# Kernel tuning notes

Measured on AMD Instinct MI355X. Metric: run time of the kernel, lower is better.

The kernel has to match this reference:

```python
import jax, jax.numpy as jnp
import numpy as np

N, E, G = 100000, 400000, 2000   # nodes, edges, graphs
IN, H = 48, 128                  # in_channels, hidden_channels (= out_channels)
L = 6                            # num GIN layers
EPS = 1e-5                       # BatchNorm eps
SLOPE = 0.01                     # leaky_relu negative slope


def setup_inputs() -> dict:
    key = jax.random.key(0)
    ks = jax.random.split(key, 12)
    x = jax.random.normal(ks[0], (N, IN), jnp.float32)
    edge_index = jax.random.randint(ks[1], (2, E), 0, N)
    edge_attr = jax.random.normal(ks[2], (E, 4), jnp.float32)  # ignored by GINConv
    # sorted graph-assignment vector; guarantee every graph has >=1 node
    batch = jnp.sort(jnp.concatenate([jnp.arange(G),
                                      jax.random.randint(ks[3], (N - G,), 0, G)]))
    s = 0.05
    W1a = jax.random.normal(ks[4], (IN, H), jnp.float32) * s        # layer-0 MLP lin1
    W1b = jax.random.normal(ks[5], (L - 1, H, H), jnp.float32) * s  # layers 1..5 MLP lin1
    b1 = jnp.zeros((L, H), jnp.float32)
    g1 = jnp.ones((L, H), jnp.float32)    # inner BN scale
    be1 = jnp.zeros((L, H), jnp.float32)  # inner BN bias
    W2 = jax.random.normal(ks[6], (L, H, H), jnp.float32) * s       # MLP lin2
    b2 = jnp.zeros((L, H), jnp.float32)
    gn = jnp.ones((L - 1, H), jnp.float32)    # outer BN scale (layers 0..4)
    bn_b = jnp.zeros((L - 1, H), jnp.float32) # outer BN bias
    fc_w = jax.random.normal(ks[7], (2 * H, 64), jnp.float32) * s
    fc_b = jnp.zeros((64,), jnp.float32)
    fc2_w = jax.random.normal(ks[8], (64, 3), jnp.float32) * s
    fc2_b = jnp.zeros((3,), jnp.float32)
    return dict(x=x, edge_attr=edge_attr, W1a=W1a, W1b=W1b, b1=b1, g1=g1, be1=be1,
                W2=W2, b2=b2, gn=gn, bn_b=bn_b, fc_w=fc_w, fc_b=fc_b,
                fc2_w=fc2_w, fc2_b=fc2_b, edge_index=edge_index, batch=batch,
                num_graphs=G)


def _bn(h, g, b):
    # training-mode BatchNorm1d over node dim (biased variance, as torch)
    m = jnp.mean(h, axis=0)
    v = jnp.mean((h - m) ** 2, axis=0)
    return g * (h - m) * jax.lax.rsqrt(v + EPS) + b


def _lrelu(h):
    return jnp.where(h >= 0, h, SLOPE * h)


def reference(x, edge_attr, W1a, W1b, b1, g1, be1, W2, b2, gn, bn_b,
              fc_w, fc_b, fc2_w, fc2_b, edge_index, batch, num_graphs):
    del edge_attr  # GINConv does not use edge attributes
    src, dst = edge_index[0], edge_index[1]
    n = x.shape[0]
    h = x
    for l in range(L):
        # GINConv: (1 + eps) * x + sum_{j in N(i)} x_j, eps = 0
        agg = jax.ops.segment_sum(h[src], dst, num_segments=n)
        z = h + agg
        W1 = W1a if l == 0 else W1b[l - 1]
        # MLP([in, H, H]) with inner BatchNorm + leaky_relu, plain last linear
        z = _lrelu(_bn(z @ W1 + b1[l], g1[l], be1[l])) @ W2[l] + b2[l]
        if l < L - 1:  # outer norm + act, skipped on last layer
            z = _lrelu(_bn(z, gn[l], bn_b[l]))
        h = z
    # dual global pooling over ragged per-graph segments
    cnt = jax.ops.segment_sum(jnp.ones((n, 1), h.dtype), batch, num_segments=num_graphs)
    p1 = jax.ops.segment_sum(h, batch, num_segments=num_graphs) / jnp.maximum(cnt, 1.0)
    p2 = jax.ops.segment_max(h, batch, num_segments=num_graphs)
    emb = jnp.concatenate([p1, p2], axis=1)            # [G, 256]
    out = _lrelu(emb @ fc_w + fc_b) @ fc2_w + fc2_b    # [G, 3]
    return out, emb
```

## Files before the change

kernel.cpp:

```cpp
#include <hip/hip_runtime.h>
#include <stdint.h>

#define N_NODES 100000
#define N_EDGES 400000
#define N_GRAPHS 2000
#define C_IN 48
#define HD 128
#define NLAYERS 6
#define BN_EPS 1e-5f
#define NSLOPE 0.01f
#define SB 391
#define NREP 8

typedef uint16_t u16;
typedef uint32_t u32;
typedef short bf16x8 __attribute__((ext_vector_type(8)));
typedef float f32x4 __attribute__((ext_vector_type(4)));

__device__ __forceinline__ float bf2f_lo(u32 v) { return __uint_as_float(v << 16); }
__device__ __forceinline__ float bf2f_hi(u32 v) { return __uint_as_float(v & 0xffff0000u); }
__device__ __forceinline__ float bf2f(u16 h) { return __uint_as_float(((u32)h) << 16); }
__device__ __forceinline__ u16 f2bf(float f) {
    u32 u = __float_as_uint(f);
    u32 r = (u + 0x7fffu + ((u >> 16) & 1u)) >> 16;
    return (u16)r;
}
__device__ __forceinline__ u32 pack2(float a, float b) {
    return (u32)f2bf(a) | ((u32)f2bf(b) << 16);
}
__device__ __forceinline__ float lrelu(float v) { return v >= 0.f ? v : v * NSLOPE; }

__global__ __launch_bounds__(256) void detect_kernel(const u16* __restrict__ x, int* __restrict__ mode) {
    __shared__ int flag;
    if (threadIdx.x == 0) flag = 0;
    __syncthreads();
    int local = 0;
    for (int i = threadIdx.x; i < 16384; i += 256) {
        float a = fabsf(bf2f(x[i]));
        if (!(a < 1e4f)) local = 1;
    }
    if (local) flag = 1;
    __syncthreads();
    if (threadIdx.x == 0) mode[0] = flag;
}

__global__ __launch_bounds__(256) void hist_kernel(const int* __restrict__ dst, int* __restrict__ cnt) {
    int e = blockIdx.x * 256 + threadIdx.x;
    if (e < N_EDGES) atomicAdd(&cnt[dst[e]], 1);
}

__global__ __launch_bounds__(256) void scan1_kernel(const int* __restrict__ cnt, int* __restrict__ bsum) {
    __shared__ int s[256];
    const int t = threadIdx.x;
    const int i = blockIdx.x * 256 + t;
    s[t] = (i < N_NODES) ? cnt[i] : 0;
    __syncthreads();
    for (int d = 128; d > 0; d >>= 1) {
        if (t < d) s[t] += s[t + d];
        __syncthreads();
    }
    if (t == 0) bsum[blockIdx.x] = s[0];
}

__global__ __launch_bounds__(512) void scan2_kernel(int* __restrict__ bsum, int* __restrict__ row_ptr) {
    __shared__ int s[SB];
    const int t = threadIdx.x;
    if (t < SB) s[t] = bsum[t];
    __syncthreads();
    if (t == 0) {
        int run = 0;
        for (int b = 0; b < SB; ++b) { int v = s[b]; s[b] = run; run += v; }
        row_ptr[0] = 0;
    }
    __syncthreads();
    if (t < SB) bsum[t] = s[t];
}

__global__ __launch_bounds__(256) void scan3_kernel(const int* __restrict__ cnt, const int* __restrict__ bsum,
                                                    int* __restrict__ row_ptr) {
    __shared__ int s[256];
    const int t = threadIdx.x;
    const int i = blockIdx.x * 256 + t;
    s[t] = (i < N_NODES) ? cnt[i] : 0;
    __syncthreads();
    if (t == 0) {
        int run = bsum[blockIdx.x];
        for (int j = 0; j < 256; ++j) { run += s[j]; s[j] = run; }
    }
    __syncthreads();
    if (i < N_NODES) row_ptr[i + 1] = s[t];
}

__global__ __launch_bounds__(256) void fill_kernel(const int* __restrict__ src, const int* __restrict__ dst,
                                                   int* __restrict__ cursor, int* __restrict__ col_idx) {
    int e = blockIdx.x * 256 + threadIdx.x;
    if (e < N_EDGES) {
        int d = dst[e];
        int slot = atomicAdd(&cursor[d], 1);
        col_idx[slot] = src[e];
    }
}

__global__ __launch_bounds__(256) void pack_w_kernel(const void* __restrict__ W1a, const void* __restrict__ W1b,
                                                     const void* __restrict__ W2, const int* __restrict__ mode,
                                                     u16* __restrict__ wpack) {
    const int t = blockIdx.x * 256 + threadIdx.x;
    if (t >= 24576) return;
    const int mat = t >> 11;
    const int r = t & 2047;
    const int l = r & 63;
    const int f = r >> 6;
    const int kb = f >> 3, nt = f & 7;
    const int k0 = kb * 32 + (l >> 4) * 8;
    const int n = nt * 16 + (l & 15);
    const int md = *mode;
    u16 vals[8];
    #pragma unroll
    for (int j = 0; j < 8; ++j) {
        const int k = k0 + j;
        float v;
        if (mat == 0) {
            v = (k < C_IN) ? (md ? ((const float*)W1a)[k * HD + n] : bf2f(((const u16*)W1a)[k * HD + n])) : 0.f;
        } else if (mat < 6) {
            const size_t o = (size_t)(mat - 1) * HD * HD + (size_t)k * HD + n;
            v = md ? ((const float*)W1b)[o] : bf2f(((const u16*)W1b)[o]);
        } else {
            const size_t o = (size_t)(mat - 6) * HD * HD + (size_t)k * HD + n;
            v = md ? ((const float*)W2)[o] : bf2f(((const u16*)W2)[o]);
        }
        vals[j] = f2bf(v);
    }
    uint4 o;
    o.x = (u32)vals[0] | ((u32)vals[1] << 16);
    o.y = (u32)vals[2] | ((u32)vals[3] << 16);
    o.z = (u32)vals[4] | ((u32)vals[5] << 16);
    o.w = (u32)vals[6] | ((u32)vals[7] << 16);
    *reinterpret_cast<uint4*>(wpack + (size_t)t * 8) = o;
}

__global__ __launch_bounds__(256) void pack_b_kernel(const void* __restrict__ b1, const void* __restrict__ b2,
                                                     const int* __restrict__ mode, float* __restrict__ biasf) {
    const int i = blockIdx.x * 256 + threadIdx.x;
    if (i >= 12 * HD) return;
    const int mat = i >> 7, c = i & 127;
    const int md = *mode;
    float v;
    if (mat < 6) v = md ? ((const float*)b1)[mat * HD + c] : bf2f(((const u16*)b1)[mat * HD + c]);
    else         v = md ? ((const float*)b2)[(mat - 6) * HD + c] : bf2f(((const u16*)b2)[(mat - 6) * HD + c]);
    biasf[i] = v;
}

__device__ __forceinline__ void coef_to_lds(float* coefs, const float* __restrict__ instats,
                                            const void* __restrict__ gammav, const void* __restrict__ betav,
                                            size_t gelem, int md, int tid) {
    if (tid < 128) {
        float sm = 0.f, sq = 0.f;
        #pragma unroll
        for (int rep = 0; rep < NREP; ++rep) {
            sm += instats[rep * 256 + tid];
            sq += instats[rep * 256 + 128 + tid];
        }
        const float inv_n = 1.0f / (float)N_NODES;
        const float mean = sm * inv_n;
        const float var = fmaxf(sq * inv_n - mean * mean, 0.f);
        const float rs = rsqrtf(var + BN_EPS);
        const float g  = md ? ((const float*)gammav)[gelem + tid] : bf2f(((const u16*)gammav)[gelem + tid]);
        const float be = md ? ((const float*)betav)[gelem + tid]  : bf2f(((const u16*)betav)[gelem + tid]);
        const float A = g * rs;
        coefs[tid] = A;
        coefs[128 + tid] = be - A * mean;
    }
}

template <int TRANS, int STATS>
__global__ __launch_bounds__(256) void gemm_mfma(const u16* A, const u16* __restrict__ wp,
                                                 const float* __restrict__ biasf,
                                                 const float* __restrict__ instats,
                                                 const void* __restrict__ gammav, const void* __restrict__ betav,
                                                 size_t gelem, const int* __restrict__ mode,
                                                 u16* out, float* __restrict__ stats) {
    __shared__ u16 Asm[32][136];
    __shared__ float sred[2][128];
    __shared__ float sqred[2][128];
    __shared__ float coefs[256];
    const int tid = threadIdx.x;
    const int m0 = blockIdx.x * 32;
    const int rrow = tid >> 4;
    const int seg = tid & 15;

    if (TRANS) {
        coef_to_lds(coefs, instats, gammav, betav, gelem, *mode, tid);
        __syncthreads();
    }

    {
        float cA[8], cB[8];
        if (TRANS) {
            #pragma unroll
            for (int j = 0; j < 8; ++j) {
                cA[j] = coefs[seg * 8 + j];
                cB[j] = coefs[128 + seg * 8 + j];
            }
        }
        uint4 v[2];
        #pragma unroll
        for (int i = 0; i < 2; ++i) {
            const int gm = m0 + i * 16 + rrow;
            if (gm < N_NODES) v[i] = *reinterpret_cast<const uint4*>(A + (size_t)gm * HD + seg * 8);
            else { v[i].x = 0; v[i].y = 0; v[i].z = 0; v[i].w = 0; }
        }
        #pragma unroll
        for (int i = 0; i < 2; ++i) {
            uint4 o = v[i];
            if (TRANS) {
                u32 w[4] = {o.x, o.y, o.z, o.w};
                #pragma unroll
                for (int p = 0; p < 4; ++p) {
                    const float lo = lrelu(cA[2 * p] * bf2f_lo(w[p]) + cB[2 * p]);
                    const float hi = lrelu(cA[2 * p + 1] * bf2f_hi(w[p]) + cB[2 * p + 1]);
                    w[p] = pack2(lo, hi);
                }
                o.x = w[0]; o.y = w[1]; o.z = w[2]; o.w = w[3];
            }
            *reinterpret_cast<uint4*>(&Asm[i * 16 + rrow][seg * 8]) = o;
        }
    }
    __syncthreads();

    const int wave = tid >> 6, lane = tid & 63;
    const int quad = lane >> 4, lx = lane & 15;
    const int rowhalf = wave & 1;
    const int colhalf = wave >> 1;
    const int wrow = rowhalf * 16;
    f32x4 acc[4] = {};
    #pragma unroll
    for (int kb = 0; kb < 4; ++kb) {
        bf16x8 bfr[4];
        #pragma unroll
        for (int nt = 0; nt < 4; ++nt)
            bfr[nt] = *reinterpret_cast<const bf16x8*>(wp + (((size_t)(kb * 8 + colhalf * 4 + nt) * 64 + lane) << 3));
        const bf16x8 af = *reinterpret_cast<const bf16x8*>(&Asm[wrow + lx][kb * 32 + quad * 8]);
        #pragma unroll
        for (int nt = 0; nt < 4; ++nt)
            acc[nt] = __builtin_amdgcn_mfma_f32_16x16x32_bf16(af, bfr[nt], acc[nt], 0, 0, 0);
    }

    const int mrow0 = m0 + wrow;
    #pragma unroll
    for (int nt = 0; nt < 4; ++nt) {
        const int n = colhalf * 64 + nt * 16 + lx;
        const float bj = biasf[n];
        float s = 0.f, q = 0.f;
        #pragma unroll
        for (int r = 0; r < 4; ++r) {
            const int m = mrow0 + quad * 4 + r;
            if (m < N_NODES) {
                const float v = acc[nt][r] + bj;
                out[(size_t)m * HD + n] = f2bf(v);
                if (STATS) { s += v; q += v * v; }
            }
        }
        if (STATS) {
            s += __shfl_xor(s, 16); s += __shfl_xor(s, 32);
            q += __shfl_xor(q, 16); q += __shfl_xor(q, 32);
            if (quad == 0) { sred[rowhalf][n] = s; sqred[rowhalf][n] = q; }
        }
    }
    if (STATS) {
        __syncthreads();
        float* sdst = stats + (size_t)(blockIdx.x & (NREP - 1)) * 256;
        if (tid < 128) {
            atomicAdd(&sdst[tid], sred[0][tid] + sred[1][tid]);
        } else if (tid < 256) {
            const int c2 = tid - 128;
            atomicAdd(&sdst[128 + c2], sqred[0][c2] + sqred[1][c2]);
        }
    }
}

__global__ __launch_bounds__(256) void gemm_gather(const u16* __restrict__ U, const int* __restrict__ row_ptr,
                                                   const int* __restrict__ col_idx, const u16* __restrict__ wp,
                                                   const float* __restrict__ biasf,
                                                   const float* __restrict__ instats,
                                                   const void* __restrict__ gammav, const void* __restrict__ betav,
                                                   size_t gelem, const int* __restrict__ mode,
                                                   u16* __restrict__ out, float* __restrict__ stats) {
    __shared__ u16 Asm[16][136];
    __shared__ float sred[128];
    __shared__ float sqred[128];
    __shared__ float coefs[256];
    const int tid = threadIdx.x;
    const int m0 = blockIdx.x * 16;
    const int rrow = tid >> 4;
    const int seg = tid & 15;

    coef_to_lds(coefs, instats, gammav, betav, gelem, *mode, tid);
    __syncthreads();

    {
        float cA[8], cB[8];
        #pragma unroll
        for (int j = 0; j < 8; ++j) {
            cA[j] = coefs[seg * 8 + j];
            cB[j] = coefs[128 + seg * 8 + j];
        }
        const int gm = m0 + rrow;
        float a[8];
        #pragma unroll
        for (int j = 0; j < 8; ++j) a[j] = 0.f;
        if (gm < N_NODES) {
            const uint4 v = *reinterpret_cast<const uint4*>(U + (size_t)gm * HD + seg * 8);
            const u32 w[4] = {v.x, v.y, v.z, v.w};
            #pragma unroll
            for (int p = 0; p < 4; ++p) {
                a[2 * p]     = lrelu(cA[2 * p] * bf2f_lo(w[p]) + cB[2 * p]);
                a[2 * p + 1] = lrelu(cA[2 * p + 1] * bf2f_hi(w[p]) + cB[2 * p + 1]);
            }
            const int s = row_ptr[gm];
            const int deg = row_ptr[gm + 1] - s;
            for (int t = 0; t < deg; t += 2) {
                const int id0 = col_idx[s + t];
                const bool h1 = (t + 1) < deg;
                const int id1 = h1 ? col_idx[s + t + 1] : 0;
                const uint4 r0 = *reinterpret_cast<const uint4*>(U + (size_t)id0 * HD + seg * 8);
                uint4 r1; r1.x = r1.y = r1.z = r1.w = 0;
                if (h1) r1 = *reinterpret_cast<const uint4*>(U + (size_t)id1 * HD + seg * 8);
                const u32 w0[4] = {r0.x, r0.y, r0.z, r0.w};
                const u32 w1[4] = {r1.x, r1.y, r1.z, r1.w};
                #pragma unroll
                for (int p = 0; p < 4; ++p) {
                    a[2 * p]     += lrelu(cA[2 * p] * bf2f_lo(w0[p]) + cB[2 * p]);
                    a[2 * p + 1] += lrelu(cA[2 * p + 1] * bf2f_hi(w0[p]) + cB[2 * p + 1]);
                    if (h1) {
                        a[2 * p]     += lrelu(cA[2 * p] * bf2f_lo(w1[p]) + cB[2 * p]);
                        a[2 * p + 1] += lrelu(cA[2 * p + 1] * bf2f_hi(w1[p]) + cB[2 * p + 1]);
                    }
                }
            }
        }
        uint4 o;
        o.x = pack2(a[0], a[1]); o.y = pack2(a[2], a[3]);
        o.z = pack2(a[4], a[5]); o.w = pack2(a[6], a[7]);
        *reinterpret_cast<uint4*>(&Asm[rrow][seg * 8]) = o;
    }
    __syncthreads();

    const int wave = tid >> 6, lane = tid & 63;
    const int quad = lane >> 4, lx = lane & 15;
    f32x4 acc[2] = {};
    #pragma unroll
    for (int kb = 0; kb < 4; ++kb) {
        bf16x8 bfr[2];
        #pragma unroll
        for (int nt = 0; nt < 2; ++nt)
            bfr[nt] = *reinterpret_cast<const bf16x8*>(wp + (((size_t)(kb * 8 + wave * 2 + nt) * 64 + lane) << 3));
        const bf16x8 af = *reinterpret_cast<const bf16x8*>(&Asm[lx][kb * 32 + quad * 8]);
        #pragma unroll
        for (int nt = 0; nt < 2; ++nt)
            acc[nt] = __builtin_amdgcn_mfma_f32_16x16x32_bf16(af, bfr[nt], acc[nt], 0, 0, 0);
    }

    #pragma unroll
    for (int nt = 0; nt < 2; ++nt) {
        const int n = wave * 32 + nt * 16 + lx;
        const float bj = biasf[n];
        float s = 0.f, q = 0.f;
        #pragma unroll
        for (int r = 0; r < 4; ++r) {
            const int m = m0 + quad * 4 + r;
            if (m < N_NODES) {
                const float v = acc[nt][r] + bj;
                out[(size_t)m * HD + n] = f2bf(v);
                s += v; q += v * v;
            }
        }
        s += __shfl_xor(s, 16); s += __shfl_xor(s, 32);
        q += __shfl_xor(q, 16); q += __shfl_xor(q, 32);
        if (quad == 0) { sred[n] = s; sqred[n] = q; }
    }
    __syncthreads();
    float* sdst = stats + (size_t)(blockIdx.x & (NREP - 1)) * 256;
    if (tid < 128) {
        atomicAdd(&sdst[tid], sred[tid]);
    } else if (tid < 256) {
        const int c2 = tid - 128;
        atomicAdd(&sdst[128 + c2], sqred[c2]);
    }
}

__global__ __launch_bounds__(256) void gemm_gather0(const void* __restrict__ xv, const int* __restrict__ row_ptr,
                                                    const int* __restrict__ col_idx, const u16* __restrict__ wp,
                                                    const float* __restrict__ biasf, const int* __restrict__ mode,
                                                    u16* __restrict__ out, float* __restrict__ stats) {
    __shared__ u16 Asm[16][136];
    __shared__ float sred[128];
    __shared__ float sqred[128];
    const int tid = threadIdx.x;
    const int m0 = blockIdx.x * 16;
    const int rrow = tid >> 4;
    const int seg = tid & 15;
    const int md = *mode;
    const bool act = seg < 6;

    {
        const int gm = m0 + rrow;
        float a[8];
        #pragma unroll
        for (int j = 0; j < 8; ++j) a[j] = 0.f;
        if (gm < N_NODES && act) {
            if (md) {
                const float* xf = (const float*)xv + (size_t)gm * C_IN + seg * 8;
                const float4 v0 = reinterpret_cast<const float4*>(xf)[0];
                const float4 v1 = reinterpret_cast<const float4*>(xf)[1];
                a[0] = v0.x; a[1] = v0.y; a[2] = v0.z; a[3] = v0.w;
                a[4] = v1.x; a[5] = v1.y; a[6] = v1.z; a[7] = v1.w;
            } else {
                const uint4 v = *reinterpret_cast<const uint4*>((const u16*)xv + (size_t)gm * C_IN + seg * 8);
                const u32 w[4] = {v.x, v.y, v.z, v.w};
                #pragma unroll
                for (int p = 0; p < 4; ++p) { a[2 * p] = bf2f_lo(w[p]); a[2 * p + 1] = bf2f_hi(w[p]); }
            }
        }
        if (gm < N_NODES) {
            const int s = row_ptr[gm];
            const int deg = row_ptr[gm + 1] - s;
            for (int t = 0; t < deg; t += 2) {
                const int id0 = col_idx[s + t];
                const bool h1 = (t + 1) < deg;
                const int id1 = h1 ? col_idx[s + t + 1] : 0;
                if (act) {
                    if (md) {
                        const float* p0 = (const float*)xv + (size_t)id0 * C_IN + seg * 8;
                        const float4 u0 = reinterpret_cast<const float4*>(p0)[0];
                        const float4 u1 = reinterpret_cast<const float4*>(p0)[1];
                        a[0] += u0.x; a[1] += u0.y; a[2] += u0.z; a[3] += u0.w;
                        a[4] += u1.x; a[5] += u1.y; a[6] += u1.z; a[7] += u1.w;
                        if (h1) {
                            const float* p1 = (const float*)xv + (size_t)id1 * C_IN + seg * 8;
                            const float4 t0 = reinterpret_cast<const float4*>(p1)[0];
                            const float4 t1 = reinterpret_cast<const float4*>(p1)[1];
                            a[0] += t0.x; a[1] += t0.y; a[2] += t0.z; a[3] += t0.w;
                            a[4] += t1.x; a[5] += t1.y; a[6] += t1.z; a[7] += t1.w;
                        }
                    } else {
                        const uint4 r0 = *reinterpret_cast<const uint4*>((const u16*)xv + (size_t)id0 * C_IN + seg * 8);
                        const u32 w0[4] = {r0.x, r0.y, r0.z, r0.w};
                        #pragma unroll
                        for (int p = 0; p < 4; ++p) { a[2 * p] += bf2f_lo(w0[p]); a[2 * p + 1] += bf2f_hi(w0[p]); }
                        if (h1) {
                            const uint4 r1 = *reinterpret_cast<const uint4*>((const u16*)xv + (size_t)id1 * C_IN + seg * 8);
                            const u32 w1[4] = {r1.x, r1.y, r1.z, r1.w};
                            #pragma unroll
                            for (int p = 0; p < 4; ++p) { a[2 * p] += bf2f_lo(w1[p]); a[2 * p + 1] += bf2f_hi(w1[p]); }
                        }
                    }
                }
            }
        }
        uint4 o;
        o.x = pack2(a[0], a[1]); o.y = pack2(a[2], a[3]);
        o.z = pack2(a[4], a[5]); o.w = pack2(a[6], a[7]);
        *reinterpret_cast<uint4*>(&Asm[rrow][seg * 8]) = o;
    }
    __syncthreads();

    const int wave = tid >> 6, lane = tid & 63;
    const int quad = lane >> 4, lx = lane & 15;
    f32x4 acc[2] = {};
    #pragma unroll
    for (int kb = 0; kb < 4; ++kb) {
        bf16x8 bfr[2];
        #pragma unroll
        for (int nt = 0; nt < 2; ++nt)
            bfr[nt] = *reinterpret_cast<const bf16x8*>(wp + (((size_t)(kb * 8 + wave * 2 + nt) * 64 + lane) << 3));
        const bf16x8 af = *reinterpret_cast<const bf16x8*>(&Asm[lx][kb * 32 + quad * 8]);
        #pragma unroll
        for (int nt = 0; nt < 2; ++nt)
            acc[nt] = __builtin_amdgcn_mfma_f32_16x16x32_bf16(af, bfr[nt], acc[nt], 0, 0, 0);
    }

    #pragma unroll
    for (int nt = 0; nt < 2; ++nt) {
        const int n = wave * 32 + nt * 16 + lx;
        const float bj = biasf[n];
        float s = 0.f, q = 0.f;
        #pragma unroll
        for (int r = 0; r < 4; ++r) {
            const int m = m0 + quad * 4 + r;
            if (m < N_NODES) {
                const float v = acc[nt][r] + bj;
                out[(size_t)m * HD + n] = f2bf(v);
                s += v; q += v * v;
            }
        }
        s += __shfl_xor(s, 16); s += __shfl_xor(s, 32);
        q += __shfl_xor(q, 16); q += __shfl_xor(q, 32);
        if (quad == 0) { sred[n] = s; sqred[n] = q; }
    }
    __syncthreads();
    float* sdst = stats + (size_t)(blockIdx.x & (NREP - 1)) * 256;
    if (tid < 128) {
        atomicAdd(&sdst[tid], sred[tid]);
    } else if (tid < 256) {
        const int c2 = tid - 128;
        atomicAdd(&sdst[128 + c2], sqred[c2]);
    }
}

__global__ __launch_bounds__(256) void pool_kernel(const u16* __restrict__ hf, const int* __restrict__ batch,
                                                   const int* __restrict__ mode, float* __restrict__ emb,
                                                   void* __restrict__ outv) {
    const int wave = threadIdx.x >> 6, lane = threadIdx.x & 63;
    const int g = blockIdx.x * 4 + wave;
    if (g >= N_GRAPHS) return;
    const int md = *mode;
    const int quad = lane >> 4, c = lane & 15;
    int lo = 0, hi = N_NODES;
    while (lo < hi) { int m = (lo + hi) >> 1; if (batch[m] < g) lo = m + 1; else hi = m; }
    const int s = lo;
    hi = N_NODES;
    while (lo < hi) { int m = (lo + hi) >> 1; if (batch[m] < g + 1) lo = m + 1; else hi = m; }
    const int e = lo;
    const int cnt = e - s;
    float sum[8], mx[8];
    #pragma unroll
    for (int j = 0; j < 8; ++j) { sum[j] = 0.f; mx[j] = -INFINITY; }
    for (int n = s + quad; n < e; n += 4) {
        const uint4 v = *reinterpret_cast<const uint4*>(hf + (size_t)n * HD + c * 8);
        const u32 w[4] = {v.x, v.y, v.z, v.w};
        #pragma unroll
        for (int p = 0; p < 4; ++p) {
            const float f0 = bf2f_lo(w[p]), f1 = bf2f_hi(w[p]);
            sum[2 * p] += f0; sum[2 * p + 1] += f1;
            mx[2 * p] = fmaxf(mx[2 * p], f0); mx[2 * p + 1] = fmaxf(mx[2 * p + 1], f1);
        }
    }
    #pragma unroll
    for (int j = 0; j < 8; ++j) {
        sum[j] += __shfl_xor(sum[j], 16); sum[j] += __shfl_xor(sum[j], 32);
        mx[j] = fmaxf(mx[j], __shfl_xor(mx[j], 16));
        mx[j] = fmaxf(mx[j], __shfl_xor(mx[j], 32));
    }
    if (quad == 0) {
        const float invc = 1.0f / (float)max(cnt, 1);
        const size_t base = (size_t)N_GRAPHS * 3 + (size_t)g * 256;
        #pragma unroll
        for (int j = 0; j < 8; ++j) {
            const float mean = sum[j] * invc;
            const float m2 = (cnt == 0) ? 0.f : mx[j];
            const int col = c * 8 + j;
            emb[(size_t)g * 256 + col] = mean;
            emb[(size_t)g * 256 + 128 + col] = m2;
            if (md) {
                ((float*)outv)[base + col] = mean;
                ((float*)outv)[base + 128 + col] = m2;
            } else {
                ((u16*)outv)[base + col] = f2bf(mean);
                ((u16*)outv)[base + 128 + col] = f2bf(m2);
            }
        }
    }
}

__global__ __launch_bounds__(64) void final_kernel(const float* __restrict__ emb, const void* __restrict__ fcwv,
                                                   const void* __restrict__ fcbv, const void* __restrict__ fc2wv,
                                                   const void* __restrict__ fc2bv, const int* __restrict__ mode,
                                                   void* __restrict__ outv) {
    __shared__ float es[256];
    __shared__ float hs[64];
    const int g = blockIdx.x, t = threadIdx.x;
    const int md = *mode;
    reinterpret_cast<float4*>(es)[t] = reinterpret_cast<const float4*>(emb + (size_t)g * 256)[t];
    __syncthreads();
    float acc = md ? ((const float*)fcbv)[t] : bf2f(((const u16*)fcbv)[t]);
    if (md) {
        const float* w = (const float*)fcwv;
        #pragma unroll 8
        for (int k = 0; k < 256; ++k) acc += es[k] * w[k * 64 + t];
    } else {
        const u16* w = (const u16*)fcwv;
        #pragma unroll 8
        for (int k = 0; k < 256; ++k) acc += es[k] * bf2f(w[k * 64 + t]);
    }
    hs[t] = lrelu(acc);
    __syncthreads();
    if (t < 3) {
        float o = md ? ((const float*)fc2bv)[t] : bf2f(((const u16*)fc2bv)[t]);
        if (md) {
            const float* w = (const float*)fc2wv;
            #pragma unroll 8
            for (int j = 0; j < 64; ++j) o += hs[j] * w[j * 3 + t];
            ((float*)outv)[(size_t)g * 3 + t] = o;
        } else {
            const u16* w = (const u16*)fc2wv;
            #pragma unroll 8
            for (int j = 0; j < 64; ++j) o += hs[j] * bf2f(w[j * 3 + t]);
            ((u16*)outv)[(size_t)g * 3 + t] = f2bf(o);
        }
    }
}

static inline size_t align256(size_t x) { return (x + 255) & ~(size_t)255; }

extern "C" void kernel_launch(void* const* d_in, const int* in_sizes, int n_in,
                              void* d_out, int out_size, void* d_ws, size_t ws_size,
                              hipStream_t stream) {
    (void)in_sizes; (void)n_in; (void)out_size; (void)ws_size;
    const void* x    = d_in[0];
    const void* W1a  = d_in[2];
    const void* W1b  = d_in[3];
    const void* b1   = d_in[4];
    const void* g1   = d_in[5];
    const void* be1  = d_in[6];
    const void* W2   = d_in[7];
    const void* b2   = d_in[8];
    const void* gn   = d_in[9];
    const void* bnb  = d_in[10];
    const void* fcw  = d_in[11];
    const void* fcb  = d_in[12];
    const void* fc2w = d_in[13];
    const void* fc2b = d_in[14];
    const int* ei    = (const int*)d_in[15];
    const int* batch = (const int*)d_in[16];

    char* p = (char*)d_ws;
    size_t off = 0;
    u16* zb = (u16*)(p + off); off += align256((size_t)N_NODES * HD * 2);
    u16* hb = (u16*)(p + off); off += align256((size_t)N_NODES * HD * 2);
    u16* wpack = (u16*)(p + off); off += align256((size_t)12 * HD * HD * 2);
    float* biasf = (float*)(p + off); off += align256((size_t)12 * HD * 4);
    float* emb = (float*)(p + off); off += align256((size_t)N_GRAPHS * 256 * 4);
    int* row_ptr = (int*)(p + off); off += align256((size_t)(N_NODES + 1) * 4);
    int* cursor = (int*)(p + off); off += align256((size_t)N_NODES * 4);
    int* col_idx = (int*)(p + off); off += align256((size_t)N_EDGES * 4);
    int* bsum = (int*)(p + off); off += align256((size_t)SB * 4);
    float* statsAll = (float*)(p + off); off += align256((size_t)12 * NREP * 256 * 4);
    int* mode = (int*)(p + off); off += align256(4);

    const int EB = (N_EDGES + 255) / 256;
    const int GBM = (N_NODES + 31) / 32;
    const int GBG = (N_NODES + 15) / 16;

    detect_kernel<<<1, 256, 0, stream>>>((const u16*)x, mode);

    hipMemsetAsync(cursor, 0, (size_t)N_NODES * 4, stream);
    hipMemsetAsync(statsAll, 0, (size_t)12 * NREP * 256 * 4, stream);
    hist_kernel<<<EB, 256, 0, stream>>>(ei + N_EDGES, cursor);
    scan1_kernel<<<SB, 256, 0, stream>>>(cursor, bsum);
    scan2_kernel<<<1, 512, 0, stream>>>(bsum, row_ptr);
    scan3_kernel<<<SB, 256, 0, stream>>>(cursor, bsum, row_ptr);
    hipMemcpyAsync(cursor, row_ptr, (size_t)N_NODES * 4, hipMemcpyDeviceToDevice, stream);
    fill_kernel<<<EB, 256, 0, stream>>>(ei, ei + N_EDGES, cursor, col_idx);
    pack_w_kernel<<<96, 256, 0, stream>>>(W1a, W1b, W2, mode, wpack);
    pack_b_kernel<<<6, 256, 0, stream>>>(b1, b2, mode, biasf);

    u16* cur = zb;
    u16* oth = hb;
    for (int l = 0; l < NLAYERS; ++l) {
        float* statsA = statsAll + (size_t)l * NREP * 256;
        float* statsB = statsAll + (size_t)(6 + l) * NREP * 256;
        float* statsBprev = statsAll + (size_t)(6 + l - 1) * NREP * 256;
        if (l == 0) {
            gemm_gather0<<<GBG, 256, 0, stream>>>(x, row_ptr, col_idx, wpack,
                                                  biasf, mode, cur, statsA);
        } else {
            gemm_gather<<<GBG, 256, 0, stream>>>(cur, row_ptr, col_idx,
                                                 wpack + (size_t)l * HD * HD,
                                                 biasf + (size_t)l * HD, statsBprev, gn, bnb,
                                                 (size_t)(l - 1) * HD, mode, oth, statsA);
            u16* t = cur; cur = oth; oth = t;
        }
        if (l < NLAYERS - 1) {
            gemm_mfma<1, 1><<<GBM, 256, 0, stream>>>(cur, wpack + (size_t)(6 + l) * HD * HD,
                                                     biasf + (size_t)(6 + l) * HD, statsA, g1, be1,
                                                     (size_t)l * HD, mode, cur, statsB);
        } else {
            gemm_mfma<1, 0><<<GBM, 256, 0, stream>>>(cur, wpack + (size_t)(6 + l) * HD * HD,
                                                     biasf + (size_t)(6 + l) * HD, statsA, g1, be1,
                                                     (size_t)l * HD, mode, cur, nullptr);
        }
    }

    pool_kernel<<<(N_GRAPHS + 3) / 4, 256, 0, stream>>>(cur, batch, mode, emb, d_out);
    final_kernel<<<N_GRAPHS, 64, 0, stream>>>(emb, fcw, fcb, fc2w, fc2b, mode, d_out);
}
```

Before: 598.2 us.

## Process gather rows in degree-sorted order to balance work per block

Adds a counting-sort pass that builds a node permutation ordered by in-degree, and the fused gather+GEMM kernels process rows in that order so nodes of similar degree share a block and a wave. This is meant to reduce divergence and tail imbalance in the neighbor-gather loops. Outputs are scattered back to original row positions, so the stores are no longer contiguous. The change also rewrites the address arithmetic to 32-bit byte offsets and uses a max-based leaky ReLU. Three small setup kernels are added.

```diff
diff --git a/kernel.cpp b/kernel.cpp
--- a/kernel.cpp
+++ b/kernel.cpp
@@ -11,6 +11,7 @@
 #define NSLOPE 0.01f
 #define SB 391
 #define NREP 8
+#define DMAX 64
 
 typedef uint16_t u16;
 typedef uint32_t u32;
@@ -28,7 +29,7 @@
 __device__ __forceinline__ u32 pack2(float a, float b) {
     return (u32)f2bf(a) | ((u32)f2bf(b) << 16);
 }
-__device__ __forceinline__ float lrelu(float v) { return v >= 0.f ? v : v * NSLOPE; }
+__device__ __forceinline__ float lrelu(float v) { return fmaxf(v * NSLOPE, v); }
 
 __global__ __launch_bounds__(256) void detect_kernel(const u16* __restrict__ x, int* __restrict__ mode) {
     __shared__ int flag;
@@ -99,6 +100,48 @@
         int slot = atomicAdd(&cursor[d], 1);
         col_idx[slot] = src[e];
     }
+}
+
+__global__ __launch_bounds__(256) void dhist_kernel(const int* __restrict__ row_ptr, int* __restrict__ dh) {
+    __shared__ int lh[DMAX];
+    const int t = threadIdx.x;
+    if (t < DMAX) lh[t] = 0;
+    __syncthreads();
+    const int i = blockIdx.x * 256 + t;
+    if (i < N_NODES) {
+        int d = row_ptr[i + 1] - row_ptr[i];
+        if (d > DMAX - 1) d = DMAX - 1;
+        atomicAdd(&lh[d], 1);
+    }
+    __syncthreads();
+    if (t < DMAX && lh[t]) atomicAdd(&dh[t], lh[t]);
+}
+
+__global__ __launch_bounds__(64) void dscan_kernel(int* __restrict__ dh, int* __restrict__ dcur) {
+    if (threadIdx.x == 0) {
+        int run = 0;
+        for (int d = DMAX - 1; d >= 0; --d) { int v = dh[d]; dh[d] = run; dcur[d] = run; run += v; }
+    }
+}
+
+__global__ __launch_bounds__(256) void dscat_kernel(const int* __restrict__ row_ptr, int* __restrict__ dcur,
+                                                    int* __restrict__ perm) {
+    __shared__ int lh[DMAX];
+    __shared__ int lbase[DMAX];
+    const int t = threadIdx.x;
+    if (t < DMAX) lh[t] = 0;
+    __syncthreads();
+    const int i = blockIdx.x * 256 + t;
+    int d = 0, r = 0;
+    if (i < N_NODES) {
+        d = row_ptr[i + 1] - row_ptr[i];
+        if (d > DMAX - 1) d = DMAX - 1;
+        r = atomicAdd(&lh[d], 1);
+    }
+    __syncthreads();
+    if (t < DMAX) lbase[t] = lh[t] ? atomicAdd(&dcur[t], lh[t]) : 0;
+    __syncthreads();
+    if (i < N_NODES) perm[lbase[d] + r] = i;
 }
 
 __global__ __launch_bounds__(256) void pack_w_kernel(const void* __restrict__ W1a, const void* __restrict__ W1b,
@@ -279,7 +322,8 @@
 }
 
 __global__ __launch_bounds__(256) void gemm_gather(const u16* __restrict__ U, const int* __restrict__ row_ptr,
-                                                   const int* __restrict__ col_idx, const u16* __restrict__ wp,
+                                                   const int* __restrict__ col_idx, const int* __restrict__ perm,
+                                                   const u16* __restrict__ wp,
                                                    const float* __restrict__ biasf,
                                                    const float* __restrict__ instats,
                                                    const void* __restrict__ gammav, const void* __restrict__ betav,
@@ -304,17 +348,21 @@
             cA[j] = coefs[seg * 8 + j];
             cB[j] = coefs[128 + seg * 8 + j];
         }
-        const int gm = m0 + rrow;
+        const int gm0 = m0 + rrow;
+        const int gm = (gm0 < N_NODES) ? perm[gm0] : -1;
         float a[8];
         #pragma unroll
         for (int j = 0; j < 8; ++j) a[j] = 0.f;
-        if (gm < N_NODES) {
-            const uint4 v = *reinterpret_cast<const uint4*>(U + (size_t)gm * HD + seg * 8);
-            const u32 w[4] = {v.x, v.y, v.z, v.w};
-            #pragma unroll
-            for (int p = 0; p < 4; ++p) {
-                a[2 * p]     = lrelu(cA[2 * p] * bf2f_lo(w[p]) + cB[2 * p]);
-                a[2 * p + 1] = lrelu(cA[2 * p + 1] * bf2f_hi(w[p]) + cB[2 * p + 1]);
+        if (gm >= 0) {
+            const u32 soff = (u32)seg << 4;
+            {
+                const uint4 v = *reinterpret_cast<const uint4*>((const char*)U + (((u32)gm << 8) + soff));
+                const u32 w[4] = {v.x, v.y, v.z, v.w};
+                #pragma unroll
+                for (int p = 0; p < 4; ++p) {
+                    a[2 * p]     = lrelu(cA[2 * p] * bf2f_lo(w[p]) + cB[2 * p]);
+                    a[2 * p + 1] = lrelu(cA[2 * p + 1] * bf2f_hi(w[p]) + cB[2 * p + 1]);
+                }
             }
             const int s = row_ptr[gm];
             const int deg = row_ptr[gm + 1] - s;
@@ -322,9 +370,9 @@
                 const int id0 = col_idx[s + t];
                 const bool h1 = (t + 1) < deg;
                 const int id1 = h1 ? col_idx[s + t + 1] : 0;
-                const uint4 r0 = *reinterpret_cast<const uint4*>(U + (size_t)id0 * HD + seg * 8);
+                const uint4 r0 = *reinterpret_cast<const uint4*>((const char*)U + (((u32)id0 << 8) + soff));
                 uint4 r1; r1.x = r1.y = r1.z = r1.w = 0;
-                if (h1) r1 = *reinterpret_cast<const uint4*>(U + (size_t)id1 * HD + seg * 8);
+                if (h1) r1 = *reinterpret_cast<const uint4*>((const char*)U + (((u32)id1 << 8) + soff));
                 const u32 w0[4] = {r0.x, r0.y, r0.z, r0.w};
                 const u32 w1[4] = {r1.x, r1.y, r1.z, r1.w};
                 #pragma unroll
@@ -360,6 +408,12 @@
             acc[nt] = __builtin_amdgcn_mfma_f32_16x16x32_bf16(af, bfr[nt], acc[nt], 0, 0, 0);
     }
 
+    int pm[4];
+    #pragma unroll
+    for (int r = 0; r < 4; ++r) {
+        const int mm = m0 + quad * 4 + r;
+        pm[r] = (mm < N_NODES) ? perm[mm] : -1;
+    }
     #pragma unroll
     for (int nt = 0; nt < 2; ++nt) {
         const int n = wave * 32 + nt * 16 + lx;
@@ -367,10 +421,9 @@
         float s = 0.f, q = 0.f;
         #pragma unroll
         for (int r = 0; r < 4; ++r) {
-            const int m = m0 + quad * 4 + r;
-            if (m < N_NODES) {
+            if (pm[r] >= 0) {
                 const float v = acc[nt][r] + bj;
-                out[(size_t)m * HD + n] = f2bf(v);
+                out[(size_t)pm[r] * HD + n] = f2bf(v);
                 s += v; q += v * v;
             }
         }
@@ -389,7 +442,8 @@
 }
 
 __global__ __launch_bounds__(256) void gemm_gather0(const void* __restrict__ xv, const int* __restrict__ row_ptr,
-                                                    const int* __restrict__ col_idx, const u16* __restrict__ wp,
+                                                    const int* __restrict__ col_idx, const int* __restrict__ perm,
+                                                    const u16* __restrict__ wp,
                                                     const float* __restrict__ biasf, const int* __restrict__ mode,
                                                     u16* __restrict__ out, float* __restrict__ stats) {
     __shared__ u16 Asm[16][136];
@@ -403,56 +457,61 @@
     const bool act = seg < 6;
 
     {
-        const int gm = m0 + rrow;
+        const int gm0 = m0 + rrow;
+        const int gm = (gm0 < N_NODES) ? perm[gm0] : -1;
         float a[8];
         #pragma unroll
         for (int j = 0; j < 8; ++j) a[j] = 0.f;
-        if (gm < N_NODES && act) {
-            if (md) {
-                const float* xf = (const float*)xv + (size_t)gm * C_IN + seg * 8;
-                const float4 v0 = reinterpret_cast<const float4*>(xf)[0];
-                const float4 v1 = reinterpret_cast<const float4*>(xf)[1];
-                a[0] = v0.x; a[1] = v0.y; a[2] = v0.z; a[3] = v0.w;
-                a[4] = v1.x; a[5] = v1.y; a[6] = v1.z; a[7] = v1.w;
-            } else {
-                const uint4 v = *reinterpret_cast<const uint4*>((const u16*)xv + (size_t)gm * C_IN + seg * 8);
-                const u32 w[4] = {v.x, v.y, v.z, v.w};
-                #pragma unroll
-                for (int p = 0; p < 4; ++p) { a[2 * p] = bf2f_lo(w[p]); a[2 * p + 1] = bf2f_hi(w[p]); }
-            }
-        }
-        if (gm < N_NODES) {
+        if (gm >= 0 && act) {
             const int s = row_ptr[gm];
             const int deg = row_ptr[gm + 1] - s;
-            for (int t = 0; t < deg; t += 2) {
-                const int id0 = col_idx[s + t];
-                const bool h1 = (t + 1) < deg;
-                const int id1 = h1 ? col_idx[s + t + 1] : 0;
-                if (act) {
-                    if (md) {
-                        const float* p0 = (const float*)xv + (size_t)id0 * C_IN + seg * 8;
-                        const float4 u0 = reinterpret_cast<const float4*>(p0)[0];
-                        const float4 u1 = reinterpret_cast<const float4*>(p0)[1];
-                        a[0] += u0.x; a[1] += u0.y; a[2] += u0.z; a[3] += u0.w;
-                        a[4] += u1.x; a[5] += u1.y; a[6] += u1.z; a[7] += u1.w;
-                        if (h1) {
-                            const float* p1 = (const float*)xv + (size_t)id1 * C_IN + seg * 8;
-                            const float4 t0 = reinterpret_cast<const float4*>(p1)[0];
-                            const float4 t1 = reinterpret_cast<const float4*>(p1)[1];
-                            a[0] += t0.x; a[1] += t0.y; a[2] += t0.z; a[3] += t0.w;
-                            a[4] += t1.x; a[5] += t1.y; a[6] += t1.z; a[7] += t1.w;
-                        }
-                    } else {
-                        const uint4 r0 = *reinterpret_cast<const uint4*>((const u16*)xv + (size_t)id0 * C_IN + seg * 8);
-                        const u32 w0[4] = {r0.x, r0.y, r0.z, r0.w};
+            if (md) {
+                const u32 soff = (u32)seg << 5;
+                {
+                    const char* pr = (const char*)xv + ((u32)gm * 192u + soff);
+                    const float4 v0 = reinterpret_cast<const float4*>(pr)[0];
+                    const float4 v1 = reinterpret_cast<const float4*>(pr)[1];
+                    a[0] = v0.x; a[1] = v0.y; a[2] = v0.z; a[3] = v0.w;
+                    a[4] = v1.x; a[5] = v1.y; a[6] = v1.z; a[7] = v1.w;
+                }
+                for (int t = 0; t < deg; t += 2) {
+                    const int id0 = col_idx[s + t];
+                    const bool h1 = (t + 1) < deg;
+                    const int id1 = h1 ? col_idx[s + t + 1] : 0;
+                    const char* p0 = (const char*)xv + ((u32)id0 * 192u + soff);
+                    const float4 u0 = reinterpret_cast<const float4*>(p0)[0];
+                    const float4 u1 = reinterpret_cast<const float4*>(p0)[1];
+                    a[0] += u0.x; a[1] += u0.y; a[2] += u0.z; a[3] += u0.w;
+                    a[4] += u1.x; a[5] += u1.y; a[6] += u1.z; a[7] += u1.w;
+                    if (h1) {
+                        const char* p1 = (const char*)xv + ((u32)id1 * 192u + soff);
+                        const float4 t0 = reinterpret_cast<const float4*>(p1)[0];
+                        const float4 t1 = reinterpret_cast<const float4*>(p1)[1];
+                        a[0] += t0.x; a[1] += t0.y; a[2] += t0.z; a[3] += t0.w;
+                        a[4] += t1.x; a[5] += t1.y; a[6] += t1.z; a[7] += t1.w;
+                    }
+                }
+            } else {
+                const u32 soff = (u32)seg << 4;
+                {
+                    const uint4 v = *reinterpret_cast<const uint4*>((const char*)xv + ((u32)gm * 96u + soff));
+                    const u32 w[4] = {v.x, v.y, v.z, v.w};
+                    #pragma unroll
+                    for (int p = 0; p < 4; ++p) { a[2 * p] = bf2f_lo(w[p]); a[2 * p + 1] = bf2f_hi(w[p]); }
+                }
+                for (int t = 0; t < deg; t += 2) {
+                    const int id0 = col_idx[s + t];
+                    const bool h1 = (t + 1) < deg;
+                    const int id1 = h1 ? col_idx[s + t + 1] : 0;
+                    const uint4 r0 = *reinterpret_cast<const uint4*>((const char*)xv + ((u32)id0 * 96u + soff));
+                    const u32 w0[4] = {r0.x, r0.y, r0.z, r0.w};
+                    #pragma unroll
+                    for (int p = 0; p < 4; ++p) { a[2 * p] += bf2f_lo(w0[p]); a[2 * p + 1] += bf2f_hi(w0[p]); }
+                    if (h1) {
+                        const uint4 r1 = *reinterpret_cast<const uint4*>((const char*)xv + ((u32)id1 * 96u + soff));
+                        const u32 w1[4] = {r1.x, r1.y, r1.z, r1.w};
                         #pragma unroll
-                        for (int p = 0; p < 4; ++p) { a[2 * p] += bf2f_lo(w0[p]); a[2 * p + 1] += bf2f_hi(w0[p]); }
-                        if (h1) {
-                            const uint4 r1 = *reinterpret_cast<const uint4*>((const u16*)xv + (size_t)id1 * C_IN + seg * 8);
-                            const u32 w1[4] = {r1.x, r1.y, r1.z, r1.w};
-                            #pragma unroll
-                            for (int p = 0; p < 4; ++p) { a[2 * p] += bf2f_lo(w1[p]); a[2 * p + 1] += bf2f_hi(w1[p]); }
-                        }
+                        for (int p = 0; p < 4; ++p) { a[2 * p] += bf2f_lo(w1[p]); a[2 * p + 1] += bf2f_hi(w1[p]); }
                     }
                 }
             }
@@ -479,6 +538,12 @@
             acc[nt] = __builtin_amdgcn_mfma_f32_16x16x32_bf16(af, bfr[nt], acc[nt], 0, 0, 0);
     }
 
+    int pm[4];
+    #pragma unroll
+    for (int r = 0; r < 4; ++r) {
+        const int mm = m0 + quad * 4 + r;
+        pm[r] = (mm < N_NODES) ? perm[mm] : -1;
+    }
     #pragma unroll
     for (int nt = 0; nt < 2; ++nt) {
         const int n = wave * 32 + nt * 16 + lx;
@@ -486,10 +551,9 @@
         float s = 0.f, q = 0.f;
         #pragma unroll
         for (int r = 0; r < 4; ++r) {
-            const int m = m0 + quad * 4 + r;
-            if (m < N_NODES) {
+            if (pm[r] >= 0) {
                 const float v = acc[nt][r] + bj;
-                out[(size_t)m * HD + n] = f2bf(v);
+                out[(size_t)pm[r] * HD + n] = f2bf(v);
                 s += v; q += v * v;
             }
         }
@@ -635,6 +699,9 @@
     int* col_idx = (int*)(p + off); off += align256((size_t)N_EDGES * 4);
     int* bsum = (int*)(p + off); off += align256((size_t)SB * 4);
     float* statsAll = (float*)(p + off); off += align256((size_t)12 * NREP * 256 * 4);
+    int* perm = (int*)(p + off); off += align256((size_t)N_NODES * 4);
+    int* dh = (int*)(p + off); off += align256((size_t)DMAX * 4);
+    int* dcur = (int*)(p + off); off += align256((size_t)DMAX * 4);
     int* mode = (int*)(p + off); off += align256(4);
 
     const int EB = (N_EDGES + 255) / 256;
@@ -645,10 +712,14 @@
 
     hipMemsetAsync(cursor, 0, (size_t)N_NODES * 4, stream);
     hipMemsetAsync(statsAll, 0, (size_t)12 * NREP * 256 * 4, stream);
+    hipMemsetAsync(dh, 0, (size_t)DMAX * 4, stream);
     hist_kernel<<<EB, 256, 0, stream>>>(ei + N_EDGES, cursor);
     scan1_kernel<<<SB, 256, 0, stream>>>(cursor, bsum);
     scan2_kernel<<<1, 512, 0, stream>>>(bsum, row_ptr);
     scan3_kernel<<<SB, 256, 0, stream>>>(cursor, bsum, row_ptr);
+    dhist_kernel<<<SB, 256, 0, stream>>>(row_ptr, dh);
+    dscan_kernel<<<1, 64, 0, stream>>>(dh, dcur);
+    dscat_kernel<<<SB, 256, 0, stream>>>(row_ptr, dcur, perm);
     hipMemcpyAsync(cursor, row_ptr, (size_t)N_NODES * 4, hipMemcpyDeviceToDevice, stream);
     fill_kernel<<<EB, 256, 0, stream>>>(ei, ei + N_EDGES, cursor, col_idx);
     pack_w_kernel<<<96, 256, 0, stream>>>(W1a, W1b, W2, mode, wpack);
@@ -661,10 +732,10 @@
         float* statsB = statsAll + (size_t)(6 + l) * NREP * 256;
         float* statsBprev = statsAll + (size_t)(6 + l - 1) * NREP * 256;
         if (l == 0) {
-            gemm_gather0<<<GBG, 256, 0, stream>>>(x, row_ptr, col_idx, wpack,
+            gemm_gather0<<<GBG, 256, 0, stream>>>(x, row_ptr, col_idx, perm, wpack,
                                                   biasf, mode, cur, statsA);
         } else {
-            gemm_gather<<<GBG, 256, 0, stream>>>(cur, row_ptr, col_idx,
+            gemm_gather<<<GBG, 256, 0, stream>>>(cur, row_ptr, col_idx, perm,
                                                  wpack + (size_t)l * HD * HD,
                                                  biasf + (size_t)l * HD, statsBprev, gn, bnb,
                                                  (size_t)(l - 1) * HD, mode, oth, statsA);
```

Result: slower. 638.3 us (+6.7%).

## Shrink dense GEMM tile to 16 rows, drop bounds checks, use 32-bit offsets

Applied to the files above, without the earlier changes.

The dense MFMA GEMM now processes 16 rows per block instead of 32, with each wave owning 32 output columns. This doubles the grid size and halves per-wave accumulators. Row bounds checks are removed from all GEMM and gather kernels because N is divisible by 16. Address arithmetic switches to 32-bit byte offsets, and leaky ReLU becomes a max. The smaller tile costs twice as many weight fragment loads per row in exchange for more parallelism and fewer registers.

```diff
diff --git a/kernel.cpp b/kernel.cpp
--- a/kernel.cpp
+++ b/kernel.cpp
@@ -28,7 +28,7 @@
 __device__ __forceinline__ u32 pack2(float a, float b) {
     return (u32)f2bf(a) | ((u32)f2bf(b) << 16);
 }
-__device__ __forceinline__ float lrelu(float v) { return v >= 0.f ? v : v * NSLOPE; }
+__device__ __forceinline__ float lrelu(float v) { return fmaxf(v * NSLOPE, v); }
 
 __global__ __launch_bounds__(256) void detect_kernel(const u16* __restrict__ x, int* __restrict__ mode) {
     __shared__ int flag;
@@ -179,12 +179,12 @@
                                                  const void* __restrict__ gammav, const void* __restrict__ betav,
                                                  size_t gelem, const int* __restrict__ mode,
                                                  u16* out, float* __restrict__ stats) {
-    __shared__ u16 Asm[32][136];
-    __shared__ float sred[2][128];
-    __shared__ float sqred[2][128];
+    __shared__ u16 Asm[16][136];
+    __shared__ float sred[128];
+    __shared__ float sqred[128];
     __shared__ float coefs[256];
     const int tid = threadIdx.x;
-    const int m0 = blockIdx.x * 32;
+    const int m0 = blockIdx.x * 16;
     const int rrow = tid >> 4;
     const int seg = tid & 15;
 
@@ -194,86 +194,69 @@
     }
 
     {
-        float cA[8], cB[8];
+        const int gm = m0 + rrow;
+        uint4 o = *reinterpret_cast<const uint4*>((const char*)A + (((u32)gm << 8) + ((u32)seg << 4)));
         if (TRANS) {
+            float cA[8], cB[8];
             #pragma unroll
             for (int j = 0; j < 8; ++j) {
                 cA[j] = coefs[seg * 8 + j];
                 cB[j] = coefs[128 + seg * 8 + j];
             }
-        }
-        uint4 v[2];
-        #pragma unroll
-        for (int i = 0; i < 2; ++i) {
-            const int gm = m0 + i * 16 + rrow;
-            if (gm < N_NODES) v[i] = *reinterpret_cast<const uint4*>(A + (size_t)gm * HD + seg * 8);
-            else { v[i].x = 0; v[i].y = 0; v[i].z = 0; v[i].w = 0; }
-        }
-        #pragma unroll
-        for (int i = 0; i < 2; ++i) {
-            uint4 o = v[i];
-            if (TRANS) {
-                u32 w[4] = {o.x, o.y, o.z, o.w};
-                #pragma unroll
-                for (int p = 0; p < 4; ++p) {
-                    const float lo = lrelu(cA[2 * p] * bf2f_lo(w[p]) + cB[2 * p]);
-                    const float hi = lrelu(cA[2 * p + 1] * bf2f_hi(w[p]) + cB[2 * p + 1]);
-                    w[p] = pack2(lo, hi);
-                }
-                o.x = w[0]; o.y = w[1]; o.z = w[2]; o.w = w[3];
+            u32 w[4] = {o.x, o.y, o.z, o.w};
+            #pragma unroll
+            for (int p = 0; p < 4; ++p) {
+                const float lo = lrelu(cA[2 * p] * bf2f_lo(w[p]) + cB[2 * p]);
+                const float hi = lrelu(cA[2 * p + 1] * bf2f_hi(w[p]) + cB[2 * p + 1]);
+                w[p] = pack2(lo, hi);
             }
-            *reinterpret_cast<uint4*>(&Asm[i * 16 + rrow][seg * 8]) = o;
-        }
+            o.x = w[0]; o.y = w[1]; o.z = w[2]; o.w = w[3];
+        }
+        *reinterpret_cast<uint4*>(&Asm[rrow][seg * 8]) = o;
     }
     __syncthreads();
 
     const int wave = tid >> 6, lane = tid & 63;
     const int quad = lane >> 4, lx = lane & 15;
-    const int rowhalf = wave & 1;
-    const int colhalf = wave >> 1;
-    const int wrow = rowhalf * 16;
-    f32x4 acc[4] = {};
+    f32x4 acc[2] = {};
     #pragma unroll
     for (int kb = 0; kb < 4; ++kb) {
-        bf16x8 bfr[4];
-        #pragma unroll
-        for (int nt = 0; nt < 4; ++nt)
-            bfr[nt] = *reinterpret_cast<const bf16x8*>(wp + (((size_t)(kb * 8 + colhalf * 4 + nt) * 64 + lane) << 3));
-        const bf16x8 af = *reinterpret_cast<const bf16x8*>(&Asm[wrow + lx][kb * 32 + quad * 8]);
-        #pragma unroll
-        for (int nt = 0; nt < 4; ++nt)
+        bf16x8 bfr[2];
+        #pragma unroll
+        for (int nt = 0; nt < 2; ++nt)
+            bfr[nt] = *reinterpret_cast<const bf16x8*>(wp + (((size_t)(kb * 8 + wave * 2 + nt) * 64 + lane) << 3));
+        const bf16x8 af = *reinterpret_cast<const bf16x8*>(&Asm[lx][kb * 32 + quad * 8]);
+        #pragma unroll
+        for (int nt = 0; nt < 2; ++nt)
             acc[nt] = __builtin_amdgcn_mfma_f32_16x16x32_bf16(af, bfr[nt], acc[nt], 0, 0, 0);
     }
 
-    const int mrow0 = m0 + wrow;
-    #pragma unroll
-    for (int nt = 0; nt < 4; ++nt) {
-        const int n = colhalf * 64 + nt * 16 + lx;
+    #pragma unroll
+    for (int nt = 0; nt < 2; ++nt) {
+        const int n = wave * 32 + nt * 16 + lx;
         const float bj = biasf[n];
         float s = 0.f, q = 0.f;
         #pragma unroll
         for (int r = 0; r < 4; ++r) {
-            const int m = mrow0 + quad * 4 + r;
-            if (m < N_NODES) {
-                const float v = acc[nt][r] + bj;
-                out[(size_t)m * HD + n] = f2bf(v);
-                if (STATS) { s += v; q += v * v; }
-            }
+            const int m = m0 + quad * 4 + r;
+            const float v = acc[nt][r] + bj;
+            out[(size_t)m * HD + n] = f2bf(v);
+            if (STATS) { s += v; q += v * v; }
         }
         if (STATS) {
             s += __shfl_xor(s, 16); s += __shfl_xor(s, 32);
             q += __shfl_xor(q, 16); q += __shfl_xor(q, 32);
-            if (quad == 0) { sred[rowhalf][n] = s; sqred[rowhalf][n] = q; }
+            if (quad == 0) { sred[n] = s; sqred[n] = q; }
         }
     }
     if (STATS) {
         __syncthreads();
         float* sdst = stats + (size_t)(blockIdx.x & (NREP - 1)) * 256;
         if (tid < 128) {
-            atomicAdd(&sdst[tid], sred[0][tid] + sred[1][tid]);
+            atomicAdd(&sdst[tid], sred[tid]);
         } else if (tid < 256) {
             const int c2 = tid - 128;
-            atomicAdd(&sdst[128 + c2], sqred[0][c2] + sqred[1][c2]);
+            atomicAdd(&sdst[128 + c2], sqred[c2]);
         }
     }
 }
@@ -305,16 +288,19 @@
             cB[j] = coefs[128 + seg * 8 + j];
         }
         const int gm = m0 + rrow;
+        const u32 soff = (u32)seg << 4;
         float a[8];
         #pragma unroll
         for (int j = 0; j < 8; ++j) a[j] = 0.f;
-        if (gm < N_NODES) {
-            const uint4 v = *reinterpret_cast<const uint4*>(U + (size_t)gm * HD + seg * 8);
-            const u32 w[4] = {v.x, v.y, v.z, v.w};
-            #pragma unroll
-            for (int p = 0; p < 4; ++p) {
-                a[2 * p]     = lrelu(cA[2 * p] * bf2f_lo(w[p]) + cB[2 * p]);
-                a[2 * p + 1] = lrelu(cA[2 * p + 1] * bf2f_hi(w[p]) + cB[2 * p + 1]);
+        {
+            {
+                const uint4 v = *reinterpret_cast<const uint4*>((const char*)U + (((u32)gm << 8) + soff));
+                const u32 w[4] = {v.x, v.y, v.z, v.w};
+                #pragma unroll
+                for (int p = 0; p < 4; ++p) {
+                    a[2 * p]     = lrelu(cA[2 * p] * bf2f_lo(w[p]) + cB[2 * p]);
+                    a[2 * p + 1] = lrelu(cA[2 * p + 1] * bf2f_hi(w[p]) + cB[2 * p + 1]);
+                }
             }
             const int s = row_ptr[gm];
             const int deg = row_ptr[gm + 1] - s;
@@ -322,9 +308,9 @@
                 const int id0 = col_idx[s + t];
                 const bool h1 = (t + 1) < deg;
                 const int id1 = h1 ? col_idx[s + t + 1] : 0;
-                const uint4 r0 = *reinterpret_cast<const uint4*>(U + (size_t)id0 * HD + seg * 8);
+                const uint4 r0 = *reinterpret_cast<const uint4*>((const char*)U + (((u32)id0 << 8) + soff));
                 uint4 r1; r1.x = r1.y = r1.z = r1.w = 0;
-                if (h1) r1 = *reinterpret_cast<const uint4*>(U + (size_t)id1 * HD + seg * 8);
+                if (h1) r1 = *reinterpret_cast<const uint4*>((const char*)U + (((u32)id1 << 8) + soff));
                 const u32 w0[4] = {r0.x, r0.y, r0.z, r0.w};
                 const u32 w1[4] = {r1.x, r1.y, r1.z, r1.w};
                 #pragma unroll
@@ -368,11 +354,9 @@
         #pragma unroll
         for (int r = 0; r < 4; ++r) {
             const int m = m0 + quad * 4 + r;
-            if (m < N_NODES) {
-                const float v = acc[nt][r] + bj;
-                out[(size_t)m * HD + n] = f2bf(v);
-                s += v; q += v * v;
-            }
+            const float v = acc[nt][r] + bj;
+            out[(size_t)m * HD + n] = f2bf(v);
+            s += v; q += v * v;
         }
         s += __shfl_xor(s, 16); s += __shfl_xor(s, 32);
         q += __shfl_xor(q, 16); q += __shfl_xor(q, 32);
@@ -407,52 +391,56 @@
         float a[8];
         #pragma unroll
         for (int j = 0; j < 8; ++j) a[j] = 0.f;
-        if (gm < N_NODES && act) {
-            if (md) {
-                const float* xf = (const float*)xv + (size_t)gm * C_IN + seg * 8;
-                const float4 v0 = reinterpret_cast<const float4*>(xf)[0];
-                const float4 v1 = reinterpret_cast<const float4*>(xf)[1];
-                a[0] = v0.x; a[1] = v0.y; a[2] = v0.z; a[3] = v0.w;
-                a[4] = v1.x; a[5] = v1.y; a[6] = v1.z; a[7] = v1.w;
-            } else {
-                const uint4 v = *reinterpret_cast<const uint4*>((const u16*)xv + (size_t)gm * C_IN + seg * 8);
-                const u32 w[4] = {v.x, v.y, v.z, v.w};
-                #pragma unroll
-                for (int p = 0; p < 4; ++p) { a[2 * p] = bf2f_lo(w[p]); a[2 * p + 1] = bf2f_hi(w[p]); }
-            }
-        }
-        if (gm < N_NODES) {
+        if (act) {
             const int s = row_ptr[gm];
             const int deg = row_ptr[gm + 1] - s;
-            for (int t = 0; t < deg; t += 2) {
-                const int id0 = col_idx[s + t];
-                const bool h1 = (t + 1) < deg;
-                const int id1 = h1 ? col_idx[s + t + 1] : 0;
-                if (act) {
-                    if (md) {
-                        const float* p0 = (const float*)xv + (size_t)id0 * C_IN + seg * 8;
-                        const float4 u0 = reinterpret_cast<const float4*>(p0)[0];
-                        const float4 u1 = reinterpret_cast<const float4*>(p0)[1];
-                        a[0] += u0.x; a[1] += u0.y; a[2] += u0.z; a[3] += u0.w;
-                        a[4] += u1.x; a[5] += u1.y; a[6] += u1.z; a[7] += u1.w;
-                        if (h1) {
-                            const float* p1 = (const float*)xv + (size_t)id1 * C_IN + seg * 8;
-                            const float4 t0 = reinterpret_cast<const float4*>(p1)[0];
-                            const float4 t1 = reinterpret_cast<const float4*>(p1)[1];
-                            a[0] += t0.x; a[1] += t0.y; a[2] += t0.z; a[3] += t0.w;
-                            a[4] += t1.x; a[5] += t1.y; a[6] += t1.z; a[7] += t1.w;
-                        }
-                    } else {
-                        const uint4 r0 = *reinterpret_cast<const uint4*>((const u16*)xv + (size_t)id0 * C_IN + seg * 8);
-                        const u32 w0[4] = {r0.x, r0.y, r0.z, r0.w};
+            if (md) {
+                const u32 soff = (u32)seg << 5;
+                {
+                    const char* pr = (const char*)xv + ((u32)gm * 192u + soff);
+                    const float4 v0 = reinterpret_cast<const float4*>(pr)[0];
+                    const float4 v1 = reinterpret_cast<const float4*>(pr)[1];
+                    a[0] = v0.x; a[1] = v0.y; a[2] = v0.z; a[3] = v0.w;
+                    a[4] = v1.x; a[5] = v1.y; a[6] = v1.z; a[7] = v1.w;
+                }
+                for (int t = 0; t < deg; t += 2) {
+                    const int id0 = col_idx[s + t];
+                    const bool h1 = (t + 1) < deg;
+                    const int id1 = h1 ? col_idx[s + t + 1] : 0;
+                    const char* p0 = (const char*)xv + ((u32)id0 * 192u + soff);
+                    const float4 u0 = reinterpret_cast<const float4*>(p0)[0];
+                    const float4 u1 = reinterpret_cast<const float4*>(p0)[1];
+                    a[0] += u0.x; a[1] += u0.y; a[2] += u0.z; a[3] += u0.w;
+                    a[4] += u1.x; a[5] += u1.y; a[6] += u1.z; a[7] += u1.w;
+                    if (h1) {
+                        const char* p1 = (const char*)xv + ((u32)id1 * 192u + soff);
+                        const float4 t0 = reinterpret_cast<const float4*>(p1)[0];
+                        const float4 t1 = reinterpret_cast<const float4*>(p1)[1];
+                        a[0] += t0.x; a[1] += t0.y; a[2] += t0.z; a[3] += t0.w;
+                        a[4] += t1.x; a[5] += t1.y; a[6] += t1.z; a[7] += t1.w;
+                    }
+                }
+            } else {
+                const u32 soff = (u32)seg << 4;
+                {
+                    const uint4 v = *reinterpret_cast<const uint4*>((const char*)xv + ((u32)gm * 96u + soff));
+                    const u32 w[4] = {v.x, v.y, v.z, v.w};
+                    #pragma unroll
+                    for (int p = 0; p < 4; ++p) { a[2 * p] = bf2f_lo(w[p]); a[2 * p + 1] = bf2f_hi(w[p]); }
+                }
+                for (int t = 0; t < deg; t += 2) {
+                    const int id0 = col_idx[s + t];
+                    const bool h1 = (t + 1) < deg;
+                    const int id1 = h1 ? col_idx[s + t + 1] : 0;
+                    const uint4 r0 = *reinterpret_cast<const uint4*>((const char*)xv + ((u32)id0 * 96u + soff));
+                    const u32 w0[4] = {r0.x, r0.y, r0.z, r0.w};
+                    #pragma unroll
+                    for (int p = 0; p < 4; ++p) { a[2 * p] += bf2f_lo(w0[p]); a[2 * p + 1] += bf2f_hi(w0[p]); }
+                    if (h1) {
+                        const uint4 r1 = *reinterpret_cast<const uint4*>((const char*)xv + ((u32)id1 * 96u + soff));
+                        const u32 w1[4] = {r1.x, r1.y, r1.z, r1.w};
                         #pragma unroll
-                        for (int p = 0; p < 4; ++p) { a[2 * p] += bf2f_lo(w0[p]); a[2 * p + 1] += bf2f_hi(w0[p]); }
-                        if (h1) {
-                            const uint4 r1 = *reinterpret_cast<const uint4*>((const u16*)xv + (size_t)id1 * C_IN + seg * 8);
-                            const u32 w1[4] = {r1.x, r1.y, r1.z, r1.w};
-                            #pragma unroll
-                            for (int p = 0; p < 4; ++p) { a[2 * p] += bf2f_lo(w1[p]); a[2 * p + 1] += bf2f_hi(w1[p]); }
-                        }
+                        for (int p = 0; p < 4; ++p) { a[2 * p] += bf2f_lo(w1[p]); a[2 * p + 1] += bf2f_hi(w1[p]); }
                     }
                 }
             }
@@ -487,11 +475,9 @@
         #pragma unroll
         for (int r = 0; r < 4; ++r) {
             const int m = m0 + quad * 4 + r;
-            if (m < N_NODES) {
-                const float v = acc[nt][r] + bj;
-                out[(size_t)m * HD + n] = f2bf(v);
-                s += v; q += v * v;
-            }
+            const float v = acc[nt][r] + bj;
+            out[(size_t)m * HD + n] = f2bf(v);
+            s += v; q += v * v;
         }
         s += __shfl_xor(s, 16); s += __shfl_xor(s, 32);
         q += __shfl_xor(q, 16); q += __shfl_xor(q, 32);
@@ -638,7 +624,6 @@
     int* mode = (int*)(p + off); off += align256(4);
 
     const int EB = (N_EDGES + 255) / 256;
-    const int GBM = (N_NODES + 31) / 32;
     const int GBG = (N_NODES + 15) / 16;
 
     detect_kernel<<<1, 256, 0, stream>>>((const u16*)x, mode);
@@ -671,11 +656,11 @@
             u16* t = cur; cur = oth; oth = t;
         }
         if (l < NLAYERS - 1) {
-            gemm_mfma<1, 1><<<GBM, 256, 0, stream>>>(cur, wpack + (size_t)(6 + l) * HD * HD,
+            gemm_mfma<1, 1><<<GBG, 256, 0, stream>>>(cur, wpack + (size_t)(6 + l) * HD * HD,
                                                      biasf + (size_t)(6 + l) * HD, statsA, g1, be1,
                                                      (size_t)l * HD, mode, cur, statsB);
         } else {
-            gemm_mfma<1, 0><<<GBM, 256, 0, stream>>>(cur, wpack + (size_t)(6 + l) * HD * HD,
+            gemm_mfma<1, 0><<<GBG, 256, 0, stream>>>(cur, wpack + (size_t)(6 + l) * HD * HD,
                                                      biasf + (size_t)(6 + l) * HD, statsA, g1, be1,
                                                      (size_t)l * HD, mode, cur, nullptr);
         }
```

Result: faster. 574.6 us (-3.9%).
